# Kernel tuning notes

Hardware: AMD Instinct MI355X
Metric: run time of the kernel (lower is better)

## Reference

```python
import jax, jax.numpy as jnp
import numpy as np

MAX_DEPTH = 8          # inner-node depths 1..8; leaves at depth 9
LMBDA = 0.1            # args.lmbda; per-node lmbda = LMBDA * 2**(-depth)
EPS = 1e-6


def setup_inputs() -> dict:
    key = jax.random.key(0)
    ks = jax.random.split(key, 7)
    B, D, O = 16384, 2048, 1000
    n_inner = 2 ** MAX_DEPTH - 1   # 255
    n_leaf = 2 ** MAX_DEPTH       # 256
    x = jax.random.normal(ks[0], (B, D), dtype=jnp.float32)
    target = jax.random.randint(ks[1], (B,), 0, O)
    y = jax.nn.one_hot(target, O, dtype=jnp.float32)  # target_onehot
    W = jax.random.normal(ks[2], (n_inner, D), dtype=jnp.float32) / np.sqrt(D)
    b = jax.random.normal(ks[3], (n_inner,), dtype=jnp.float32) * 0.01
    beta = jax.random.normal(ks[4], (n_inner,), dtype=jnp.float32)
    leaf_params = jax.random.normal(ks[5], (n_leaf, O), dtype=jnp.float32)
    return {"x": x, "y": y, "W": W, "b": b, "beta": beta, "leaf_params": leaf_params}


def reference(x, y, W, b, beta, leaf_params):
    """Faithful vectorized version of SoftDecisionTree.cal_loss.
    Inner nodes are stored in level-order (heap) layout, left-to-right
    within each level, matching the left-first recursion of cal_prob.
    Returns (loss, output) like cal_loss.
    """
    B = x.shape[0]
    dt = x.dtype
    # All inner-node gates in one fused GEMM: sigmoid(beta * (x @ w + b))
    probs = jax.nn.sigmoid(beta * (x @ W.T + b))  # [B, n_inner]

    path = jnp.ones((B, 1), dt)  # path_prob_init
    C = jnp.asarray(0.0, dt)
    idx = 0
    for d in range(1, MAX_DEPTH + 1):  # small fixed loop over tree levels
        n = 2 ** (d - 1)
        p = probs[:, idx:idx + n]      # gate probs for this level's nodes [B, n]
        if d < MAX_DEPTH:              # get_penalty skips nodes whose children are leaves
            denom = jnp.sum(path, axis=0)                  # [n]
            denom = jnp.where(denom == 0, EPS, denom)
            alpha = jnp.sum(p * path, axis=0) / denom      # [n]
            alpha = jnp.clip(alpha, EPS, 1.0 - EPS)
            lmbda = LMBDA * 2.0 ** (-d)
            C = C - jnp.sum(lmbda * 0.5 * (jnp.log(alpha) + jnp.log1p(-alpha)))
        # children: left gets path*(1-p), right gets path*p, interleaved
        path = jnp.stack([path * (1.0 - p), path * p], axis=-1).reshape(B, 2 * n)
        idx += n
    # path: [B, n_leaf] leaf arrival probabilities (left-to-right leaf order)

    logQ = jax.nn.log_softmax(leaf_params, axis=-1)  # [n_leaf, O]
    TQ = y @ logQ.T                                  # [B, n_leaf]: y . log Q per leaf
    loss_term = jnp.mean(jnp.sum(path * TQ, axis=1))
    loss = -loss_term + C

    best = jnp.argmax(path, axis=1)   # first max, matches the '<' update order
    output = jnp.exp(logQ)[best]      # [B, O] max_Q
    return loss, output
```

## Files before the change

### kernel.cpp

```cpp
#include <hip/hip_runtime.h>


typedef __attribute__((ext_vector_type(8))) short short8;
typedef __attribute__((ext_vector_type(4))) float f32x4;

#define DIM 2048
#define NCLS 1000
#define NINNER 255
#define NPAD 256

__device__ __forceinline__ unsigned cvt2bf(float a, float b) {
  return ((__float_as_uint(a) + 0x8000u) >> 16) | ((__float_as_uint(b) + 0x8000u) & 0xFFFF0000u);
}

__device__ __forceinline__ void async_copy16(const unsigned short* gsrc, unsigned short* ldst) {
  __builtin_amdgcn_global_load_lds(
      (const __attribute__((address_space(1))) unsigned int*)(gsrc),
      (__attribute__((address_space(3))) unsigned int*)(ldst), 16, 0, 0);
}

__global__ __launch_bounds__(256) void prep_w(const float* __restrict__ W,
                                              const float* __restrict__ b,
                                              const float* __restrict__ beta,
                                              unsigned short* __restrict__ Wb,
                                              float* __restrict__ bp,
                                              float* __restrict__ betap) {
  int i = blockIdx.x * 256 + threadIdx.x;
  int n = i >> 11;
  float v = (n < NINNER) ? W[i] : 0.f;
  Wb[i] = (unsigned short)((__float_as_uint(v) + 0x8000u) >> 16);
  if (i < NPAD) {
    bp[i] = (i < NINNER) ? b[i] : 0.f;
    betap[i] = (i < NINNER) ? beta[i] : 0.f;
  }
}

__global__ __launch_bounds__(256) void leaf_softmax(const float* __restrict__ leaf,
                                                    float* __restrict__ logQT,
                                                    float* __restrict__ Q) {
  int l = blockIdx.x, t = threadIdx.x;
  const float* row = leaf + (size_t)l * NCLS;
  __shared__ float red[256];
  float mx = -3.4e38f;
  for (int j = t; j < NCLS; j += 256) mx = fmaxf(mx, row[j]);
  red[t] = mx; __syncthreads();
  for (int s = 128; s; s >>= 1) { if (t < s) red[t] = fmaxf(red[t], red[t + s]); __syncthreads(); }
  mx = red[0]; __syncthreads();
  float sm = 0.f;
  for (int j = t; j < NCLS; j += 256) sm += __expf(row[j] - mx);
  red[t] = sm; __syncthreads();
  for (int s = 128; s; s >>= 1) { if (t < s) red[t] += red[t + s]; __syncthreads(); }
  float lse = mx + __logf(red[0]);
  for (int j = t; j < NCLS; j += 256) {
    float lg = row[j] - lse;
    logQT[(size_t)j * NPAD + l] = lg;
    Q[(size_t)l * NCLS + j] = __expf(lg);
  }
}

__global__ __launch_bounds__(256) void find_targets(const float* __restrict__ y,
                                                    int* __restrict__ tgt) {
  int wv = threadIdx.x >> 6, lane = threadIdx.x & 63;
  int r = blockIdx.x * 4 + wv;
  const float4* yr = (const float4*)(y + (size_t)r * NCLS);
  int found = 0x7fffffff;
#pragma unroll
  for (int i = 0; i < 4; ++i) {
    int j4 = i * 64 + lane;
    if (j4 < 250) {
      float4 v = yr[j4];
      if (v.x > 0.5f) found = min(found, 4 * j4 + 0);
      if (v.y > 0.5f) found = min(found, 4 * j4 + 1);
      if (v.z > 0.5f) found = min(found, 4 * j4 + 2);
      if (v.w > 0.5f) found = min(found, 4 * j4 + 3);
    }
  }
  for (int off = 32; off; off >>= 1) found = min(found, __shfl_down(found, off));
  if (lane == 0) tgt[r] = found;
}

__global__ __launch_bounds__(256, 2) void gemm_xwT(const float* __restrict__ x,
                                                   const unsigned short* __restrict__ Wb,
                                                   float* __restrict__ P0,
                                                   float* __restrict__ P1) {
  __shared__ __align__(16) unsigned short As[128 * 40];
  __shared__ __align__(16) unsigned short Bs[128 * 32];

  int tid = threadIdx.x;
  int lane = tid & 63, wave = tid >> 6;
  int m_base = blockIdx.x * 128;
  int n_base = blockIdx.y * 128;
  int k_base = blockIdx.z * 1024;
  float* P = blockIdx.z ? P1 : P0;

  f32x4 acc[4][4] = {};

  int arow = tid >> 1, aseg = tid & 1;
  const float* aptr = x + (size_t)(m_base + arow) * DIM + k_base + aseg * 16;
  unsigned short* asd = &As[arow * 40 + aseg * 16];

  int ci0 = wave * 2, ci1 = wave * 2 + 1;
  const unsigned short* bg0 =
      Wb + (size_t)(n_base + ci0 * 16 + (lane >> 2)) * DIM + k_base + (lane & 3) * 8;
  const unsigned short* bg1 = bg0 + (size_t)16 * DIM;
  unsigned short* bl0 = &Bs[ci0 * 512];
  unsigned short* bl1 = &Bs[ci1 * 512];

  int frow = lane & 15, fquad = lane >> 4;
  int wrow = (wave & 1) * 64;
  int wcol = (wave >> 1) * 64;

  for (int kt = 0; kt < 1024; kt += 32) {
    const float4* ap = (const float4*)(aptr + kt);
    float4 v0 = ap[0], v1 = ap[1], v2 = ap[2], v3 = ap[3];
    uint4 p0, p1;
    p0.x = cvt2bf(v0.x, v0.y); p0.y = cvt2bf(v0.z, v0.w);
    p0.z = cvt2bf(v1.x, v1.y); p0.w = cvt2bf(v1.z, v1.w);
    p1.x = cvt2bf(v2.x, v2.y); p1.y = cvt2bf(v2.z, v2.w);
    p1.z = cvt2bf(v3.x, v3.y); p1.w = cvt2bf(v3.z, v3.w);
    __syncthreads();
    *(uint4*)asd = p0;
    *(uint4*)(asd + 8) = p1;
    async_copy16(bg0 + kt, bl0);
    async_copy16(bg1 + kt, bl1);
    __syncthreads();
    short8 a[4];
#pragma unroll
    for (int mt = 0; mt < 4; ++mt)
      a[mt] = *(const short8*)&As[(wrow + mt * 16 + frow) * 40 + fquad * 8];
#pragma unroll
    for (int nt = 0; nt < 4; ++nt) {
      short8 bb = *(const short8*)&Bs[(wcol + nt * 16 + frow) * 32 + fquad * 8];
#pragma unroll
      for (int mt = 0; mt < 4; ++mt)
        acc[mt][nt] = __builtin_amdgcn_mfma_f32_16x16x32_bf16(a[mt], bb, acc[mt][nt], 0, 0, 0);
    }
  }
#pragma unroll
  for (int mt = 0; mt < 4; ++mt) {
#pragma unroll
    for (int rg = 0; rg < 4; ++rg) {
      float* dst = P + (size_t)(m_base + wrow + mt * 16 + fquad * 4 + rg) * NPAD + n_base + wcol + frow;
#pragma unroll
      for (int nt = 0; nt < 4; ++nt) dst[nt * 16] = acc[mt][nt][rg];
    }
  }
}

__global__ __launch_bounds__(256) void tree_walk(const float* __restrict__ P0,
                                                 const float* __restrict__ P1,
                                                 const float* __restrict__ bp,
                                                 const float* __restrict__ betap,
                                                 const float* __restrict__ logQT,
                                                 const int* __restrict__ tgt,
                                                 float* __restrict__ acc,
                                                 int* __restrict__ best) {
  __shared__ float ws[4][256];
  __shared__ float s0s[127], s1s[127];
  __shared__ float sdot;
  int tid = threadIdx.x;
  int lane = tid & 63, wv = tid >> 6;
  if (tid < 127) { s0s[tid] = 0.f; s1s[tid] = 0.f; }
  if (tid == 255) sdot = 0.f;
  __syncthreads();
  float4 bb = *(const float4*)(bp + lane * 4);
  float4 be = *(const float4*)(betap + lane * 4);
  float* wsp = ws[wv];
  float wdot = 0.f;
  for (int it = 0; it < 4; ++it) {
    int r = blockIdx.x * 16 + wv * 4 + it;
    float4 u = *(const float4*)(P0 + (size_t)r * NPAD + lane * 4);
    float4 v = *(const float4*)(P1 + (size_t)r * NPAD + lane * 4);
    float4 pz;
    pz.x = 1.f / (1.f + __expf(-be.x * (u.x + v.x + bb.x)));
    pz.y = 1.f / (1.f + __expf(-be.y * (u.y + v.y + bb.y)));
    pz.z = 1.f / (1.f + __expf(-be.z * (u.z + v.z + bb.z)));
    pz.w = 1.f / (1.f + __expf(-be.w * (u.w + v.w + bb.w)));
    *(float4*)(wsp + lane * 4) = pz;
    __asm__ volatile("" ::: "memory");
    int tg = tgt[r];
    float pp = 1.f;
#pragma unroll
    for (int d = 1; d <= 6; ++d) {
      int idx = (1 << (d - 1)) - 1 + (lane >> (7 - d));
      float p = wsp[idx];
      if ((lane & ((1 << (7 - d)) - 1)) == 0) {
        atomicAdd(&s0s[idx], pp);
        atomicAdd(&s1s[idx], p * pp);
      }
      pp *= ((lane >> (6 - d)) & 1) ? p : (1.f - p);
    }
    float p7 = wsp[63 + lane];
    atomicAdd(&s0s[63 + lane], pp);
    atomicAdd(&s1s[63 + lane], p7 * pp);
    float pL = pp * (1.f - p7), pR = pp * p7;
    float p8a = wsp[127 + 2 * lane], p8b = wsp[128 + 2 * lane];
    float lf0 = pL * (1.f - p8a), lf1 = pL * p8a;
    float lf2 = pR * (1.f - p8b), lf3 = pR * p8b;
    float4 lq = *(const float4*)(logQT + (size_t)tg * NPAD + lane * 4);
    wdot += lf0 * lq.x + lf1 * lq.y + lf2 * lq.z + lf3 * lq.w;
    float bv = lf0; int bi = 4 * lane;
    if (lf1 > bv) { bv = lf1; bi = 4 * lane + 1; }
    if (lf2 > bv) { bv = lf2; bi = 4 * lane + 2; }
    if (lf3 > bv) { bv = lf3; bi = 4 * lane + 3; }
    for (int off = 32; off; off >>= 1) {
      float ov = __shfl_down(bv, off);
      int oi = __shfl_down(bi, off);
      if (ov > bv || (ov == bv && oi < bi)) { bv = ov; bi = oi; }
    }
    if (lane == 0) best[r] = bi;
  }
  for (int off = 32; off; off >>= 1) wdot += __shfl_down(wdot, off);
  if (lane == 0) atomicAdd(&sdot, wdot);
  __syncthreads();
  if (tid < 127) {
    atomicAdd(&acc[tid], s0s[tid]);
    atomicAdd(&acc[127 + tid], s1s[tid]);
  }
  if (tid == 255) atomicAdd(&acc[254], sdot);
}

__global__ __launch_bounds__(128) void finalize_loss(const float* __restrict__ acc,
                                                     float* __restrict__ out) {
  __shared__ float red[128];
  int t = threadIdx.x;
  float c = 0.f;
  if (t < 127) {
    float denom = acc[t];
    if (denom == 0.f) denom = 1e-6f;
    float alpha = acc[127 + t] / denom;
    alpha = fminf(fmaxf(alpha, 1e-6f), 1.f - 1e-6f);
    int d = 31 - __clz(t + 1) + 1;
    float lm = 0.1f * exp2f(-(float)d);
    c = -lm * 0.5f * (logf(alpha) + log1pf(-alpha));
  }
  red[t] = c;
  __syncthreads();
  for (int s = 64; s; s >>= 1) { if (t < s) red[t] += red[t + s]; __syncthreads(); }
  if (t == 0) out[0] = -(acc[254] / 16384.f) + red[0];
}

__global__ __launch_bounds__(256) void gather_rows(const float* __restrict__ Q,
                                                   const int* __restrict__ best,
                                                   float* __restrict__ out) {
  int wv = threadIdx.x >> 6, lane = threadIdx.x & 63;
  int r = blockIdx.x * 4 + wv;
  const float* src = Q + (size_t)best[r] * NCLS;
  float* dst = out + 1 + (size_t)r * NCLS;
  if (lane < 3) dst[lane] = src[lane];
  if (lane == 0) dst[999] = src[999];
#pragma unroll
  for (int i = 0; i < 4; ++i) {
    int q = i * 64 + lane;
    if (q < 249) {
      int o = 3 + 4 * q;
      float4 v = make_float4(src[o], src[o + 1], src[o + 2], src[o + 3]);
      *(float4*)(dst + o) = v;
    }
  }
}

extern "C" void kernel_launch(void* const* d_in, const int* in_sizes, int n_in,
                              void* d_out, int out_size, void* d_ws, size_t ws_size,
                              hipStream_t stream) {
  const float* x = (const float*)d_in[0];
  const float* y = (const float*)d_in[1];
  const float* W = (const float*)d_in[2];
  const float* b = (const float*)d_in[3];
  const float* beta = (const float*)d_in[4];
  const float* leaf = (const float*)d_in[5];
  float* out = (float*)d_out;
  char* ws = (char*)d_ws;

  unsigned short* Wb = (unsigned short*)(ws + 0);
  float* bp    = (float*)(ws + 1048576);
  float* betap = (float*)(ws + 1049600);
  float* acc   = (float*)(ws + 1050624);
  int* tgt     = (int*)(ws + 1051648);
  int* best    = (int*)(ws + 1117184);
  float* logQT = (float*)(ws + 1182720);
  float* Q     = (float*)(ws + 2206720);
  float* P0    = (float*)(ws + 3230720);
  float* P1    = out + 4;

  prep_w<<<2048, 256, 0, stream>>>(W, b, beta, Wb, bp, betap);
  leaf_softmax<<<256, 256, 0, stream>>>(leaf, logQT, Q);
  find_targets<<<4096, 256, 0, stream>>>(y, tgt);
  gemm_xwT<<<dim3(128, 2, 2), 256, 0, stream>>>(x, Wb, P0, P1);
  hipMemsetAsync(acc, 0, 256 * sizeof(float), stream);
  tree_walk<<<1024, 256, 0, stream>>>(P0, P1, bp, betap, logQT, tgt, acc, best);
  finalize_loss<<<1, 128, 0, stream>>>(acc, out);
  gather_rows<<<4096, 256, 0, stream>>>(Q, best, out);
}
```

Baseline: 362.9 us.

## Fuse gate GEMM with tree walk and pre-pack W into MFMA fragment layout

The separate split-K GEMM and tree_walk kernels are merged into one kernel that computes a 32-row tile over the full K. The tile's gate logits stay in LDS and feed the sigmoid and tree traversal directly, so the P0/P1 intermediate round trip through global memory goes away. W is pre-packed into MFMA-fragment order so B fragments load straight from global memory. x is streamed as fp32 into swizzled, double-buffered LDS via async global_load_lds and converted to bf16 at fragment read. Per-level penalty sums are accumulated in registers across rows before the LDS atomics, trading more per-block work and possible L2 pressure on the W reads for fewer launches and less traffic.

New measurement: 320.2 us. -11.8%, faster.

```diff
diff --git a/kernel.cpp b/kernel.cpp
--- a/kernel.cpp
+++ b/kernel.cpp
@@ -8,12 +8,15 @@
 #define NCLS 1000
 #define NINNER 255
 #define NPAD 256
+#define BM 32
+#define CHUNKF 128
+#define NCHUNK 16
 
 __device__ __forceinline__ unsigned cvt2bf(float a, float b) {
   return ((__float_as_uint(a) + 0x8000u) >> 16) | ((__float_as_uint(b) + 0x8000u) & 0xFFFF0000u);
 }
 
-__device__ __forceinline__ void async_copy16(const unsigned short* gsrc, unsigned short* ldst) {
+__device__ __forceinline__ void async_copy16(const float* gsrc, void* ldst) {
   __builtin_amdgcn_global_load_lds(
       (const __attribute__((address_space(1))) unsigned int*)(gsrc),
       (__attribute__((address_space(3))) unsigned int*)(ldst), 16, 0, 0);
@@ -22,16 +25,27 @@
 __global__ __launch_bounds__(256) void prep_w(const float* __restrict__ W,
                                               const float* __restrict__ b,
                                               const float* __restrict__ beta,
-                                              unsigned short* __restrict__ Wb,
+                                              unsigned short* __restrict__ WbP,
                                               float* __restrict__ bp,
                                               float* __restrict__ betap) {
-  int i = blockIdx.x * 256 + threadIdx.x;
-  int n = i >> 11;
-  float v = (n < NINNER) ? W[i] : 0.f;
-  Wb[i] = (unsigned short)((__float_as_uint(v) + 0x8000u) >> 16);
-  if (i < NPAD) {
-    bp[i] = (i < NINNER) ? b[i] : 0.f;
-    betap[i] = (i < NINNER) ? beta[i] : 0.f;
+  int f = blockIdx.x * 256 + threadIdx.x;
+  int kt = f >> 10;
+  int T = (f >> 6) & 15;
+  int l = f & 63;
+  int row = T * 16 + (l & 15);
+  int k0 = kt * 32 + (l >> 4) * 8;
+  uint4 o = make_uint4(0u, 0u, 0u, 0u);
+  if (row < NINNER) {
+    const float* src = W + (size_t)row * DIM + k0;
+    o.x = cvt2bf(src[0], src[1]);
+    o.y = cvt2bf(src[2], src[3]);
+    o.z = cvt2bf(src[4], src[5]);
+    o.w = cvt2bf(src[6], src[7]);
+  }
+  *(uint4*)(WbP + (size_t)f * 8) = o;
+  if (f < NPAD) {
+    bp[f] = (f < NINNER) ? b[f] : 0.f;
+    betap[f] = (f < NINNER) ? beta[f] : 0.f;
   }
 }
 
@@ -79,120 +93,128 @@
   if (lane == 0) tgt[r] = found;
 }
 
-__global__ __launch_bounds__(256, 2) void gemm_xwT(const float* __restrict__ x,
-                                                   const unsigned short* __restrict__ Wb,
-                                                   float* __restrict__ P0,
-                                                   float* __restrict__ P1) {
-  __shared__ __align__(16) unsigned short As[128 * 40];
-  __shared__ __align__(16) unsigned short Bs[128 * 32];
+__device__ __forceinline__ void chunk_mma(f32x4 (&ac)[2][4], const float* Ab,
+                                          const unsigned short* bptr, int c,
+                                          int frow, int fq) {
+#pragma unroll
+  for (int s = 0; s < 4; ++s) {
+    int kt = c * 4 + s;
+    short8 bfr[4];
+#pragma unroll
+    for (int nt = 0; nt < 4; ++nt)
+      bfr[nt] = *(const short8*)(bptr + ((size_t)kt * 1024 + nt * 64) * 8);
+    short8 afr[2];
+#pragma unroll
+    for (int mt = 0; mt < 2; ++mt) {
+      int R = mt * 16 + frow;
+      int r7 = R & 7;
+      const float4* base = (const float4*)(Ab + R * 128 + s * 32);
+      float4 va = base[(2 * fq) ^ r7];
+      float4 vb = base[(2 * fq + 1) ^ r7];
+      union { uint4 u; short8 s8; } cv;
+      cv.u.x = cvt2bf(va.x, va.y);
+      cv.u.y = cvt2bf(va.z, va.w);
+      cv.u.z = cvt2bf(vb.x, vb.y);
+      cv.u.w = cvt2bf(vb.z, vb.w);
+      afr[mt] = cv.s8;
+    }
+#pragma unroll
+    for (int nt = 0; nt < 4; ++nt)
+#pragma unroll
+      for (int mt = 0; mt < 2; ++mt)
+        ac[mt][nt] = __builtin_amdgcn_mfma_f32_16x16x32_bf16(afr[mt], bfr[nt], ac[mt][nt], 0, 0, 0);
+  }
+}
+
+__global__ __launch_bounds__(256, 2) void gemm_tree(
+    const float* __restrict__ x, const unsigned short* __restrict__ WbP,
+    const float* __restrict__ bp, const float* __restrict__ betap,
+    const float* __restrict__ logQT, const int* __restrict__ tgt,
+    float* __restrict__ acc, int* __restrict__ best) {
+  __shared__ __align__(16) float As[2][4096];
+  __shared__ float s0s[127], s1s[127], sdot;
 
   int tid = threadIdx.x;
   int lane = tid & 63, wave = tid >> 6;
-  int m_base = blockIdx.x * 128;
-  int n_base = blockIdx.y * 128;
-  int k_base = blockIdx.z * 1024;
-  float* P = blockIdx.z ? P1 : P0;
-
-  f32x4 acc[4][4] = {};
-
-  int arow = tid >> 1, aseg = tid & 1;
-  const float* aptr = x + (size_t)(m_base + arow) * DIM + k_base + aseg * 16;
-  unsigned short* asd = &As[arow * 40 + aseg * 16];
-
-  int ci0 = wave * 2, ci1 = wave * 2 + 1;
-  const unsigned short* bg0 =
-      Wb + (size_t)(n_base + ci0 * 16 + (lane >> 2)) * DIM + k_base + (lane & 3) * 8;
-  const unsigned short* bg1 = bg0 + (size_t)16 * DIM;
-  unsigned short* bl0 = &Bs[ci0 * 512];
-  unsigned short* bl1 = &Bs[ci1 * 512];
-
-  int frow = lane & 15, fquad = lane >> 4;
-  int wrow = (wave & 1) * 64;
-  int wcol = (wave >> 1) * 64;
-
-  for (int kt = 0; kt < 1024; kt += 32) {
-    const float4* ap = (const float4*)(aptr + kt);
-    float4 v0 = ap[0], v1 = ap[1], v2 = ap[2], v3 = ap[3];
-    uint4 p0, p1;
-    p0.x = cvt2bf(v0.x, v0.y); p0.y = cvt2bf(v0.z, v0.w);
-    p0.z = cvt2bf(v1.x, v1.y); p0.w = cvt2bf(v1.z, v1.w);
-    p1.x = cvt2bf(v2.x, v2.y); p1.y = cvt2bf(v2.z, v2.w);
-    p1.z = cvt2bf(v3.x, v3.y); p1.w = cvt2bf(v3.z, v3.w);
-    __syncthreads();
-    *(uint4*)asd = p0;
-    *(uint4*)(asd + 8) = p1;
-    async_copy16(bg0 + kt, bl0);
-    async_copy16(bg1 + kt, bl1);
-    __syncthreads();
-    short8 a[4];
-#pragma unroll
-    for (int mt = 0; mt < 4; ++mt)
-      a[mt] = *(const short8*)&As[(wrow + mt * 16 + frow) * 40 + fquad * 8];
-#pragma unroll
-    for (int nt = 0; nt < 4; ++nt) {
-      short8 bb = *(const short8*)&Bs[(wcol + nt * 16 + frow) * 32 + fquad * 8];
-#pragma unroll
-      for (int mt = 0; mt < 4; ++mt)
-        acc[mt][nt] = __builtin_amdgcn_mfma_f32_16x16x32_bf16(a[mt], bb, acc[mt][nt], 0, 0, 0);
-    }
-  }
-#pragma unroll
-  for (int mt = 0; mt < 4; ++mt) {
-#pragma unroll
-    for (int rg = 0; rg < 4; ++rg) {
-      float* dst = P + (size_t)(m_base + wrow + mt * 16 + fquad * 4 + rg) * NPAD + n_base + wcol + frow;
-#pragma unroll
-      for (int nt = 0; nt < 4; ++nt) dst[nt * 16] = acc[mt][nt][rg];
-    }
-  }
-}
-
-__global__ __launch_bounds__(256) void tree_walk(const float* __restrict__ P0,
-                                                 const float* __restrict__ P1,
-                                                 const float* __restrict__ bp,
-                                                 const float* __restrict__ betap,
-                                                 const float* __restrict__ logQT,
-                                                 const int* __restrict__ tgt,
-                                                 float* __restrict__ acc,
-                                                 int* __restrict__ best) {
-  __shared__ float ws[4][256];
-  __shared__ float s0s[127], s1s[127];
-  __shared__ float sdot;
-  int tid = threadIdx.x;
-  int lane = tid & 63, wv = tid >> 6;
+  int frow = lane & 15, fq = lane >> 4;
+  int m_base = blockIdx.x * BM;
+
   if (tid < 127) { s0s[tid] = 0.f; s1s[tid] = 0.f; }
   if (tid == 255) sdot = 0.f;
-  __syncthreads();
-  float4 bb = *(const float4*)(bp + lane * 4);
-  float4 be = *(const float4*)(betap + lane * 4);
-  float* wsp = ws[wv];
+
+  const float* asrc[4];
+  int aoff[4];
+#pragma unroll
+  for (int a = 0; a < 4; ++a) {
+    int L = a * 4096 + tid * 16;
+    int r = L >> 9;
+    int j = (L >> 4) & 31;
+    int c16 = (j & 24) | ((j & 7) ^ (r & 7));
+    asrc[a] = x + (size_t)(m_base + r) * DIM + c16 * 4;
+    aoff[a] = L;
+  }
+
+  const unsigned short* bptr = WbP + ((size_t)wave * 256 + lane) * 8;
+
+  f32x4 accA[2][4] = {}, accB[2][4] = {};
+
+#pragma unroll
+  for (int a = 0; a < 4; ++a) async_copy16(asrc[a], (char*)As[0] + aoff[a]);
+  __syncthreads();
+
+  for (int c = 0; c < NCHUNK; ++c) {
+    if (c + 1 < NCHUNK) {
+      float* nb = As[(c + 1) & 1];
+#pragma unroll
+      for (int a = 0; a < 4; ++a)
+        async_copy16(asrc[a] + (c + 1) * CHUNKF, (char*)nb + aoff[a]);
+    }
+    const float* Ab = As[c & 1];
+    if (c < 8) chunk_mma(accA, Ab, bptr, c, frow, fq);
+    else       chunk_mma(accB, Ab, bptr, c, frow, fq);
+    __syncthreads();
+  }
+
+  float* Ps = &As[0][0];
+#pragma unroll
+  for (int mt = 0; mt < 2; ++mt)
+#pragma unroll
+    for (int nt = 0; nt < 4; ++nt)
+#pragma unroll
+      for (int rg = 0; rg < 4; ++rg)
+        Ps[(mt * 16 + fq * 4 + rg) * 256 + wave * 64 + nt * 16 + frow] =
+            accA[mt][nt][rg] + accB[mt][nt][rg];
+  __syncthreads();
+
+  {
+    float bc = bp[tid], bec = betap[tid];
+#pragma unroll 4
+    for (int i = 0; i < 32; ++i) {
+      float v = Ps[i * 256 + tid];
+      Ps[i * 256 + tid] = 1.f / (1.f + __expf(-bec * (v + bc)));
+    }
+  }
+  __syncthreads();
+
   float wdot = 0.f;
-  for (int it = 0; it < 4; ++it) {
-    int r = blockIdx.x * 16 + wv * 4 + it;
-    float4 u = *(const float4*)(P0 + (size_t)r * NPAD + lane * 4);
-    float4 v = *(const float4*)(P1 + (size_t)r * NPAD + lane * 4);
-    float4 pz;
-    pz.x = 1.f / (1.f + __expf(-be.x * (u.x + v.x + bb.x)));
-    pz.y = 1.f / (1.f + __expf(-be.y * (u.y + v.y + bb.y)));
-    pz.z = 1.f / (1.f + __expf(-be.z * (u.z + v.z + bb.z)));
-    pz.w = 1.f / (1.f + __expf(-be.w * (u.w + v.w + bb.w)));
-    *(float4*)(wsp + lane * 4) = pz;
-    __asm__ volatile("" ::: "memory");
+  float s0r[7] = {}, s1r[7] = {};
+  for (int it = 0; it < 8; ++it) {
+    int rl = wave * 8 + it;
+    int r = m_base + rl;
+    const float* wsp = Ps + rl * 256;
     int tg = tgt[r];
     float pp = 1.f;
 #pragma unroll
     for (int d = 1; d <= 6; ++d) {
       int idx = (1 << (d - 1)) - 1 + (lane >> (7 - d));
       float p = wsp[idx];
-      if ((lane & ((1 << (7 - d)) - 1)) == 0) {
-        atomicAdd(&s0s[idx], pp);
-        atomicAdd(&s1s[idx], p * pp);
-      }
+      s0r[d - 1] += pp;
+      s1r[d - 1] += p * pp;
       pp *= ((lane >> (6 - d)) & 1) ? p : (1.f - p);
     }
     float p7 = wsp[63 + lane];
-    atomicAdd(&s0s[63 + lane], pp);
-    atomicAdd(&s1s[63 + lane], p7 * pp);
+    s0r[6] += pp;
+    s1r[6] += p7 * pp;
     float pL = pp * (1.f - p7), pR = pp * p7;
     float p8a = wsp[127 + 2 * lane], p8b = wsp[128 + 2 * lane];
     float lf0 = pL * (1.f - p8a), lf1 = pL * p8a;
@@ -210,6 +232,16 @@
     }
     if (lane == 0) best[r] = bi;
   }
+#pragma unroll
+  for (int d = 1; d <= 6; ++d) {
+    int idx = (1 << (d - 1)) - 1 + (lane >> (7 - d));
+    if ((lane & ((1 << (7 - d)) - 1)) == 0) {
+      atomicAdd(&s0s[idx], s0r[d - 1]);
+      atomicAdd(&s1s[idx], s1r[d - 1]);
+    }
+  }
+  atomicAdd(&s0s[63 + lane], s0r[6]);
+  atomicAdd(&s1s[63 + lane], s1r[6]);
   for (int off = 32; off; off >>= 1) wdot += __shfl_down(wdot, off);
   if (lane == 0) atomicAdd(&sdot, wdot);
   __syncthreads();
@@ -272,23 +304,20 @@
   float* out = (float*)d_out;
   char* ws = (char*)d_ws;
 
-  unsigned short* Wb = (unsigned short*)(ws + 0);
+  unsigned short* WbP = (unsigned short*)(ws + 0);
   float* bp    = (float*)(ws + 1048576);
   float* betap = (float*)(ws + 1049600);
-  float* acc   = (float*)(ws + 1050624);
+  float* accb  = (float*)(ws + 1050624);
   int* tgt     = (int*)(ws + 1051648);
   int* best    = (int*)(ws + 1117184);
   float* logQT = (float*)(ws + 1182720);
   float* Q     = (float*)(ws + 2206720);
-  float* P0    = (float*)(ws + 3230720);
-  float* P1    = out + 4;
-
-  prep_w<<<2048, 256, 0, stream>>>(W, b, beta, Wb, bp, betap);
+
+  prep_w<<<256, 256, 0, stream>>>(W, b, beta, WbP, bp, betap);
   leaf_softmax<<<256, 256, 0, stream>>>(leaf, logQT, Q);
   find_targets<<<4096, 256, 0, stream>>>(y, tgt);
-  gemm_xwT<<<dim3(128, 2, 2), 256, 0, stream>>>(x, Wb, P0, P1);
-  hipMemsetAsync(acc, 0, 256 * sizeof(float), stream);
-  tree_walk<<<1024, 256, 0, stream>>>(P0, P1, bp, betap, logQT, tgt, acc, best);
-  finalize_loss<<<1, 128, 0, stream>>>(acc, out);
+  hipMemsetAsync(accb, 0, 256 * sizeof(float), stream);
+  gemm_tree<<<512, 256, 0, stream>>>(x, WbP, bp, betap, logQT, tgt, accb, best);
+  finalize_loss<<<1, 128, 0, stream>>>(accb, out);
   gather_rows<<<4096, 256, 0, stream>>>(Q, best, out);
 }
```
